# Kernel optimization log

Hardware: AMD Instinct MI355X
Metric: run time of the kernel (lower is better)

The kernel has to match this reference:

```python
import jax, jax.numpy as jnp
import numpy as np

NCLASSES = 80
MAX_BOXES = 100
IOU_THR = 0.5
SCORE_THR = 0.0
NEG = -1e9


def arrange_bbox(xy, wh):
    # xy, wh: [1, H, W, 3, 2]
    H, W = xy.shape[1], xy.shape[2]
    gx, gy = jnp.meshgrid(jnp.arange(W), jnp.arange(H))  # 'xy' indexing, each [H, W]
    grid = jnp.stack([gx, gy], axis=-1)[:, :, None, :].astype(xy.dtype)  # [H, W, 1, 2]
    gsize = jnp.array([H, W], dtype=xy.dtype)  # TF divides last dim [x, y] by [H, W]
    xy = (xy + grid) / gsize
    return jnp.concatenate([xy - wh / 2, xy + wh / 2], axis=-1)  # [1,H,W,3,4]


def hard_nms(boxes, scores):
    # boxes: [N,4] (x1,y1,x2,y2); scores: [N]. Greedy NMS, fixed MAX_BOXES output.
    areas = (boxes[:, 2] - boxes[:, 0]) * (boxes[:, 3] - boxes[:, 1])  # [N]

    def step(sw, _):
        j = jnp.argmax(sw)
        s = sw[j]
        valid = s > SCORE_THR
        bj = boxes[j]
        iw = jnp.clip(jnp.minimum(boxes[:, 2], bj[2]) - jnp.maximum(boxes[:, 0], bj[0]), 0.0)
        ih = jnp.clip(jnp.minimum(boxes[:, 3], bj[3]) - jnp.maximum(boxes[:, 1], bj[1]), 0.0)
        inter = iw * ih
        iou = inter / (areas + areas[j] - inter)
        sw = jnp.where((iou > IOU_THR) & valid, NEG, sw)  # suppresses j itself too
        return sw, (jnp.where(valid, j, -1), jnp.where(valid, s, 0.0), valid)

    _, (sel_idx, sel_scores, valids) = jax.lax.scan(step, scores, None, length=MAX_BOXES)
    return sel_idx, sel_scores, valids


def decode(grid0, grid1, grid2, anchors_table):
    outs = (grid0, grid1, grid2)
    anch = (anchors_table[2], anchors_table[1], anchors_table[0])
    bbs, confs, probs = [], [], []
    for g, a in zip(outs, anch):
        xy, wh, obj, cp = jnp.split(g, [2, 4, 5], axis=-1)
        b = arrange_bbox(xy, jnp.exp(wh) * a)
        bbs.append(b.reshape(1, -1, 4))
        confs.append(obj.reshape(1, -1, 1))
        probs.append(cp.reshape(1, -1, NCLASSES))
    bbox = jnp.concatenate(bbs, axis=1).reshape(-1, 4)          # [N,4]
    conf = jnp.concatenate(confs, axis=1)[0, :, 0]              # [N]
    cp = jnp.concatenate(probs, axis=1)[0]                      # [N,C]
    cls_idx = jnp.argmax(cp, axis=-1)                           # [N]
    maxprob = jnp.max(cp, axis=-1)                              # [N]
    # TF code broadcasts conf[1,N,1]*maxprob[N] -> [N,N], then reduce_max over axis 1.
    # Mathematically: scores[i] = max_j conf[i]*maxprob[j] = max(conf*max(mp), conf*min(mp)).
    scores = jnp.maximum(conf * jnp.max(maxprob), conf * jnp.min(maxprob))
    return bbox, scores, cls_idx


def reference(grid0, grid1, grid2, anchors_table):
    bbox, scores, cls_idx = decode(grid0, grid1, grid2, anchors_table)
    sel_idx, sel_scores, valids = hard_nms(bbox, scores)
    safe = jnp.clip(sel_idx, 0)
    sel_boxes = jnp.where(valids[:, None], bbox[safe], 0.0)[None]      # [1,MAX,4]
    sel_scores = sel_scores[None]                                       # [1,MAX]
    sel_classes = jnp.where(valids, cls_idx[safe], 0)[None]            # [1,MAX]
    num_valid = jnp.sum(valids).astype(jnp.int32)[None]                # [1]
    return sel_boxes, sel_scores, sel_classes, num_valid


def setup_inputs() -> dict:
    key = jax.random.key(0)
    k0, k1, k2 = jax.random.split(key, 3)
    grid0 = jax.random.normal(k0, (1, 48, 48, 3, 85), jnp.float32)
    grid1 = jax.random.normal(k1, (1, 96, 96, 3, 85), jnp.float32)
    grid2 = jax.random.normal(k2, (1, 192, 192, 3, 85), jnp.float32)
    anchors = np.array([[[10, 13], [16, 30], [33, 23]],
                        [[30, 61], [62, 45], [59, 119]],
                        [[116, 90], [156, 198], [373, 326]]], np.float32) / 416.0
    return {"grid0": grid0, "grid1": grid1, "grid2": grid2,
            "anchors_table": jnp.asarray(anchors)}
```

## Files before the change

kernel.cpp:

```cpp
#include <hip/hip_runtime.h>
#include <hip/hip_bf16.h>
#include <math.h>


#define NCLS  80
#define MAXB  100
#define N0    6912
#define N1    27648
#define NTOT  145152
#define NTILE 2268
#define NB    4096
#define CAP   2048
#define CAPL  2048
#define CHUNK 256
#define NEGF  -3.402823466e38f
#define POSF   3.402823466e38f

#define WS_CONF 0
#define WS_SCAL (NTOT * 4)
#define WS_PART (WS_SCAL + 16)
#define WS_HIST (WS_PART + NTILE * 16)
#define WS_BINC (WS_HIST + 8 * NB * 4)
#define WS_SUF  (WS_BINC + NB * 4)
#define WS_META (WS_SUF + (NB + 2) * 4)
#define WS_CAND (WS_META + 16)

__device__ __forceinline__ int binOf(float s, float Smax) {
    int b = (int)((s / Smax) * (float)NB);
    return b > (NB - 1) ? (NB - 1) : b;
}
__device__ __forceinline__ float smaxOf(const float* scal) {
    float Mx = scal[0], Mn = scal[1], cmx = scal[2], cmn = scal[3];
    return fmaxf(fmaxf(cmx * Mx, cmx * Mn), fmaxf(cmn * Mx, cmn * Mn));
}
__device__ __forceinline__ float rdlane(float v, int l) {
    return __uint_as_float(__builtin_amdgcn_readlane(__float_as_uint(v), l));
}
__device__ __forceinline__ void decodeBox(int idx, const float* __restrict__ g0,
        const float* __restrict__ g1, const float* __restrict__ g2,
        const float* __restrict__ anch,
        float& x1, float& y1, float& x2, float& y2) {
    const float* g; int H, ar, j;
    if (idx < N0)           { g = g0; H = 48;  ar = 2; j = idx; }
    else if (idx < N0 + N1) { g = g1; H = 96;  ar = 1; j = idx - N0; }
    else                    { g = g2; H = 192; ar = 0; j = idx - N0 - N1; }
    const float* r = g + (size_t)j * 85;
    float tx = r[0], ty = r[1], tw = r[2], th = r[3];
    int cell = j / 3, a = j - cell * 3;
    int hh = cell / H, ww = cell - hh * H;
    float xc = (tx + (float)ww) / (float)H;
    float yc = (ty + (float)hh) / (float)H;
    float bw = expf(tw) * anch[ar * 6 + a * 2];
    float bh = expf(th) * anch[ar * 6 + a * 2 + 1];
    x1 = xc - bw * 0.5f; y1 = yc - bh * 0.5f;
    x2 = xc + bw * 0.5f; y2 = yc + bh * 0.5f;
}

__global__ __launch_bounds__(256) void k_decode(
        const float* __restrict__ g0, const float* __restrict__ g1,
        const float* __restrict__ g2, float* __restrict__ conf,
        float* __restrict__ part) {
    __shared__ float sm[5440];
    __shared__ float red[16];
    const int tid = threadIdx.x;
    const int tile = blockIdx.x;
    const float* p; int ibase, lt;
    if (tile < 108)      { p = g0; ibase = 0;       lt = tile; }
    else if (tile < 540) { p = g1; ibase = N0;      lt = tile - 108; }
    else                 { p = g2; ibase = N0 + N1; lt = tile - 540; }
    const float4* src = (const float4*)(p + (size_t)lt * 5440);
    for (int w = tid; w < 1360; w += 256) ((float4*)sm)[w] = src[w];
    __syncthreads();

    const int b = tid >> 2, pp = tid & 3;
    const float* row = sm + b * 85;
    float best = row[5 + pp * 20];
    #pragma unroll
    for (int k = 1; k < 20; k++) best = fmaxf(best, row[5 + pp * 20 + k]);
    best = fmaxf(best, __shfl_xor(best, 1));
    best = fmaxf(best, __shfl_xor(best, 2));
    float cmx = NEGF, cmn = POSF;
    if (pp == 0) {
        float obj = row[4];
        conf[ibase + lt * 64 + b] = obj;
        cmx = obj; cmn = obj;
    }
    float mpmax = best, mpmin = best;
    for (int off = 32; off; off >>= 1) {
        mpmax = fmaxf(mpmax, __shfl_down(mpmax, off));
        mpmin = fminf(mpmin, __shfl_down(mpmin, off));
        cmx   = fmaxf(cmx,   __shfl_down(cmx,   off));
        cmn   = fminf(cmn,   __shfl_down(cmn,   off));
    }
    const int lane = tid & 63, wid = tid >> 6;
    if (lane == 0) {
        red[wid * 4 + 0] = mpmax; red[wid * 4 + 1] = mpmin;
        red[wid * 4 + 2] = cmx;   red[wid * 4 + 3] = cmn;
    }
    __syncthreads();
    if (tid == 0) {
        float a0 = red[0], a1 = red[1], a2 = red[2], a3 = red[3];
        for (int w = 1; w < 4; w++) {
            a0 = fmaxf(a0, red[w * 4 + 0]); a1 = fminf(a1, red[w * 4 + 1]);
            a2 = fmaxf(a2, red[w * 4 + 2]); a3 = fminf(a3, red[w * 4 + 3]);
        }
        part[tile * 4 + 0] = a0; part[tile * 4 + 1] = a1;
        part[tile * 4 + 2] = a2; part[tile * 4 + 3] = a3;
    }
}

__global__ __launch_bounds__(256) void k_reduce(const float* __restrict__ part,
                                                float* __restrict__ scal) {
    __shared__ float red[16];
    const int tid = threadIdx.x;
    float a0 = NEGF, a1 = POSF, a2 = NEGF, a3 = POSF;
    for (int b = tid; b < NTILE; b += 256) {
        float4 p4 = ((const float4*)part)[b];
        a0 = fmaxf(a0, p4.x); a1 = fminf(a1, p4.y);
        a2 = fmaxf(a2, p4.z); a3 = fminf(a3, p4.w);
    }
    for (int off = 32; off; off >>= 1) {
        a0 = fmaxf(a0, __shfl_down(a0, off)); a1 = fminf(a1, __shfl_down(a1, off));
        a2 = fmaxf(a2, __shfl_down(a2, off)); a3 = fminf(a3, __shfl_down(a3, off));
    }
    const int lane = tid & 63, wid = tid >> 6;
    if (lane == 0) {
        red[wid * 4 + 0] = a0; red[wid * 4 + 1] = a1;
        red[wid * 4 + 2] = a2; red[wid * 4 + 3] = a3;
    }
    __syncthreads();
    if (tid == 0) {
        for (int w = 1; w < 4; w++) {
            a0 = fmaxf(a0, red[w * 4 + 0]); a1 = fminf(a1, red[w * 4 + 1]);
            a2 = fmaxf(a2, red[w * 4 + 2]); a3 = fminf(a3, red[w * 4 + 3]);
        }
        scal[0] = a0; scal[1] = a1; scal[2] = a2; scal[3] = a3;
    }
}

__global__ __launch_bounds__(256) void k_hist(const float* __restrict__ conf,
                                              const float* __restrict__ scal,
                                              int* __restrict__ hist) {
    int i = blockIdx.x * 256 + threadIdx.x;
    float Mx = scal[0], Mn = scal[1];
    float Smax = smaxOf(scal);
    float c = conf[i];
    float s = fmaxf(c * Mx, c * Mn);
    if (s > 0.0f && Smax > 0.0f)
        atomicAdd(&hist[((blockIdx.x & 7) << 12) + binOf(s, Smax)], 1);
}

__global__ __launch_bounds__(1024) void k_thresh(const int* __restrict__ hist,
                                                 int* __restrict__ suf,
                                                 int* __restrict__ meta) {
    __shared__ int grp[1024];
    const int tid = threadIdx.x;
    int b0 = tid * 4;
    int h[4];
    #pragma unroll
    for (int q = 0; q < 4; q++) {
        int s = 0;
        #pragma unroll
        for (int sh = 0; sh < 8; sh++) s += hist[sh * NB + b0 + q];
        h[q] = s;
    }
    grp[tid] = h[0] + h[1] + h[2] + h[3];
    __syncthreads();
    for (int d = 1; d < 1024; d <<= 1) {
        int add = (tid + d < 1024) ? grp[tid + d] : 0;
        __syncthreads();
        grp[tid] += add;
        __syncthreads();
    }
    int gnext = (tid + 1 < 1024) ? grp[tid + 1] : 0;
    suf[b0 + 3] = gnext + h[3];
    suf[b0 + 2] = gnext + h[3] + h[2];
    suf[b0 + 1] = gnext + h[3] + h[2] + h[1];
    suf[b0 + 0] = gnext + h[3] + h[2] + h[1] + h[0];
    if (tid == 0) suf[NB] = 0;
    __syncthreads();
    if (tid == 0) {
        int L = 0, R = NB - 1, res = NB - 1;
        while (L <= R) {
            int m = (L + R) >> 1;
            if (suf[m] <= CAP) { res = m; R = m - 1; } else L = m + 1;
        }
        meta[0] = res;
    }
}

__global__ __launch_bounds__(256) void k_compact(
        const float* __restrict__ conf, const float* __restrict__ scal,
        const int* __restrict__ suf, const int* __restrict__ meta,
        int* __restrict__ binCtr, unsigned long long* __restrict__ cand) {
    int i = blockIdx.x * 256 + threadIdx.x;
    float Mx = scal[0], Mn = scal[1];
    float Smax = smaxOf(scal);
    float c = conf[i];
    float s = fmaxf(c * Mx, c * Mn);
    int lo = meta[0];
    if (s > 0.0f && Smax > 0.0f) {
        int b = binOf(s, Smax);
        if (b >= lo) {
            int pos = suf[b + 1] + atomicAdd(&binCtr[b], 1);
            if (pos < CAP)
                cand[pos] = ((unsigned long long)__float_as_uint(s) << 32)
                          | (unsigned long long)(~(unsigned)i);
        }
    }
}

__global__ __launch_bounds__(64) void k_nms(
        const float* __restrict__ g0, const float* __restrict__ g1,
        const float* __restrict__ g2, const float* __restrict__ anch,
        const float* __restrict__ conf, const float* __restrict__ scal,
        const int* __restrict__ suf, const int* __restrict__ meta,
        const unsigned long long* __restrict__ cand, float* __restrict__ out) {
    __shared__ unsigned long long keys[CAPL];
    __shared__ float selX1[MAXB], selY1[MAXB], selX2[MAXB], selY2[MAXB],
                     selA[MAXB], selS[MAXB];
    __shared__ int selIdx[MAXB];
    __shared__ int sh_cnt;

    const int lane = threadIdx.x;
    const float Mx = scal[0], Mn = scal[1];
    const float Smax = smaxOf(scal);
    const int loGlob = meta[0];
    int nsel = 0;
    int hi = NB;

    while (nsel < MAXB && hi > 0) {
        const bool fast = hi > loGlob;
        const int sufHi = suf[hi];
        int l;
        {
            int lb = fast ? loGlob : 0;
            int capHere = fast ? CHUNK : CAPL;
            int L = lb, R = hi - 1, res = hi - 1;
            while (L <= R) {
                int m = (L + R) >> 1;
                if (suf[m] - sufHi <= capHere) { res = m; R = m - 1; } else L = m + 1;
            }
            l = res;
        }
        int cnt;
        if (fast) {
            cnt = suf[l] - sufHi;
            for (int i = lane; i < cnt; i += 64) keys[i] = cand[sufHi + i];
        } else {
            if (lane == 0) sh_cnt = 0;
            __syncthreads();
            for (int i = lane; i < NTOT; i += 64) {
                float c = conf[i];
                float s = fmaxf(c * Mx, c * Mn);
                if (s > 0.0f) {
                    int b = binOf(s, Smax);
                    if (b >= l && b < hi) {
                        int pos = atomicAdd(&sh_cnt, 1);
                        if (pos < CAPL)
                            keys[pos] = ((unsigned long long)__float_as_uint(s) << 32)
                                      | (unsigned long long)(~(unsigned)i);
                    }
                }
            }
            __syncthreads();
            cnt = sh_cnt; if (cnt > CAPL) cnt = CAPL;
        }
        if (cnt > 0) {
            int n = 2; while (n < cnt) n <<= 1;
            for (int i = cnt + lane; i < n; i += 64) keys[i] = 0ULL;
            __syncthreads();
            for (int k = 2; k <= n; k <<= 1) {
                for (int j = k >> 1; j > 0; j >>= 1) {
                    int half = n >> 1;
                    for (int t = lane; t < half; t += 64) {
                        int i = ((t & ~(j - 1)) << 1) | (t & (j - 1));
                        int ixj = i | j;
                        unsigned long long ka = keys[i], kb = keys[ixj];
                        if ((ka < kb) == ((i & k) == 0)) { keys[i] = kb; keys[ixj] = ka; }
                    }
                    __syncthreads();
                }
            }
            for (int bpos = 0; bpos < cnt && nsel < MAXB; bpos += 64) {
                int t = bpos + lane;
                bool alive = (t < cnt);
                float x1 = 0.f, y1 = 0.f, x2 = 0.f, y2 = 0.f, area = 0.f, sc = 0.f;
                int idx = 0;
                if (alive) {
                    unsigned long long key = keys[t];
                    idx = (int)(~(unsigned)key);
                    sc = __uint_as_float((unsigned)(key >> 32));
                    decodeBox(idx, g0, g1, g2, anch, x1, y1, x2, y2);
                    area = (x2 - x1) * (y2 - y1);
                    for (int s2 = 0; s2 < nsel; s2++) {
                        float iw = fminf(x2, selX2[s2]) - fmaxf(x1, selX1[s2]);
                        float ih = fminf(y2, selY2[s2]) - fmaxf(y1, selY1[s2]);
                        iw = fmaxf(iw, 0.f); ih = fmaxf(ih, 0.f);
                        float inter = iw * ih;
                        if (inter / (area + selA[s2] - inter) > 0.5f) { alive = false; break; }
                    }
                }
                while (nsel < MAXB) {
                    unsigned long long bal = __ballot(alive);
                    if (!bal) break;
                    int w = __ffsll((unsigned long long)bal) - 1;
                    float wx1 = rdlane(x1, w), wy1 = rdlane(y1, w);
                    float wx2 = rdlane(x2, w), wy2 = rdlane(y2, w);
                    float wa  = rdlane(area, w);
                    if (lane == w) {
                        selX1[nsel] = x1; selY1[nsel] = y1;
                        selX2[nsel] = x2; selY2[nsel] = y2;
                        selA[nsel] = area; selS[nsel] = sc; selIdx[nsel] = idx;
                    }
                    if (alive) {
                        float iw = fminf(x2, wx2) - fmaxf(x1, wx1);
                        float ih = fminf(y2, wy2) - fmaxf(y1, wy1);
                        iw = fmaxf(iw, 0.f); ih = fmaxf(ih, 0.f);
                        float inter = iw * ih;
                        if (inter / (area + wa - inter) > 0.5f) alive = false;
                    }
                    nsel++;
                }
                __syncthreads();
            }
        }
        hi = l;
    }
    __syncthreads();

    for (int k = lane; k < MAXB; k += 64) {
        float b0 = 0.f, b1 = 0.f, b2 = 0.f, b3 = 0.f, sv = 0.f, cv = 0.f;
        if (k < nsel) {
            b0 = selX1[k]; b1 = selY1[k]; b2 = selX2[k]; b3 = selY2[k];
            sv = selS[k];
            int idx = selIdx[k];
            const float* g; int j;
            if (idx < N0)           { g = g0; j = idx; }
            else if (idx < N0 + N1) { g = g1; j = idx - N0; }
            else                    { g = g2; j = idx - N0 - N1; }
            const float* r = g + (size_t)j * 85 + 5;
            float v[NCLS];
            #pragma unroll
            for (int q = 0; q < NCLS; q++) v[q] = r[q];
            float best = v[0]; int c = 0;
            #pragma unroll
            for (int q = 1; q < NCLS; q++)
                if (v[q] > best) { best = v[q]; c = q; }
            cv = (float)c;
        }
        out[4 * k + 0] = b0; out[4 * k + 1] = b1;
        out[4 * k + 2] = b2; out[4 * k + 3] = b3;
        out[400 + k] = sv;
        out[500 + k] = cv;
    }
    if (lane == 0) out[600] = (float)nsel;
}

extern "C" void kernel_launch(void* const* d_in, const int* in_sizes, int n_in,
                              void* d_out, int out_size, void* d_ws, size_t ws_size,
                              hipStream_t stream) {
    const float* g0   = (const float*)d_in[0];
    const float* g1   = (const float*)d_in[1];
    const float* g2   = (const float*)d_in[2];
    const float* anch = (const float*)d_in[3];
    char* ws = (char*)d_ws;
    float* conf  = (float*)(ws + WS_CONF);
    float* scal  = (float*)(ws + WS_SCAL);
    float* part  = (float*)(ws + WS_PART);
    int*   hist  = (int*)(ws + WS_HIST);
    int*   binc  = (int*)(ws + WS_BINC);
    int*   suf   = (int*)(ws + WS_SUF);
    int*   meta  = (int*)(ws + WS_META);
    unsigned long long* cand = (unsigned long long*)(ws + WS_CAND);
    float* out   = (float*)d_out;

    hipMemsetAsync(ws + WS_HIST, 0, 9 * NB * 4, stream);
    k_decode <<<NTILE, 256, 0, stream>>>(g0, g1, g2, conf, part);
    k_reduce <<<1, 256, 0, stream>>>(part, scal);
    k_hist   <<<NTOT / 256, 256, 0, stream>>>(conf, scal, hist);
    k_thresh <<<1, 1024, 0, stream>>>(hist, suf, meta);
    k_compact<<<NTOT / 256, 256, 0, stream>>>(conf, scal, suf, meta, binc, cand);
    k_nms    <<<1, 64, 0, stream>>>(g0, g1, g2, anch, conf, scal, suf, meta, cand, out);
}
```

Before: 161.3 us.

## Fold memset and reduce into neighbouring kernels, precompute NMS chunk boundaries, keep selected boxes in registers

Removes the hipMemsetAsync and the single-block k_reduce launch. Histogram zeroing moves into k_decode, and each k_hist block redundantly reduces the per-tile partials itself. k_thresh now also computes the global scalars and a ladder of four thresholds (256..2048), so k_nms can load its candidate chunks directly without per-chunk binary searches. Selected boxes are held in wave registers and read with readlane instead of from shared memory. The cost is redundant partial reductions in every hist block and more register pressure in the NMS kernel.

Measured after the change: 167.2 us. 1.04x slower.

```diff
diff --git a/kernel.cpp b/kernel.cpp
--- a/kernel.cpp
+++ b/kernel.cpp
@@ -9,10 +9,10 @@
 #define N1    27648
 #define NTOT  145152
 #define NTILE 2268
+#define NHB   567
 #define NB    4096
 #define CAP   2048
 #define CAPL  2048
-#define CHUNK 256
 #define NEGF  -3.402823466e38f
 #define POSF   3.402823466e38f
 
@@ -22,16 +22,12 @@
 #define WS_HIST (WS_PART + NTILE * 16)
 #define WS_BINC (WS_HIST + 8 * NB * 4)
 #define WS_SUF  (WS_BINC + NB * 4)
-#define WS_META (WS_SUF + (NB + 2) * 4)
+#define WS_META (WS_SUF + (NB + 4) * 4)
 #define WS_CAND (WS_META + 16)
 
 __device__ __forceinline__ int binOf(float s, float Smax) {
     int b = (int)((s / Smax) * (float)NB);
     return b > (NB - 1) ? (NB - 1) : b;
-}
-__device__ __forceinline__ float smaxOf(const float* scal) {
-    float Mx = scal[0], Mn = scal[1], cmx = scal[2], cmn = scal[3];
-    return fmaxf(fmaxf(cmx * Mx, cmx * Mn), fmaxf(cmn * Mx, cmn * Mn));
 }
 __device__ __forceinline__ float rdlane(float v, int l) {
     return __uint_as_float(__builtin_amdgcn_readlane(__float_as_uint(v), l));
@@ -59,11 +55,12 @@
 __global__ __launch_bounds__(256) void k_decode(
         const float* __restrict__ g0, const float* __restrict__ g1,
         const float* __restrict__ g2, float* __restrict__ conf,
-        float* __restrict__ part) {
+        float* __restrict__ part, int* __restrict__ histAll) {
     __shared__ float sm[5440];
     __shared__ float red[16];
     const int tid = threadIdx.x;
     const int tile = blockIdx.x;
+    if (tile < 144) histAll[tile * 256 + tid] = 0;
     const float* p; int ibase, lt;
     if (tile < 108)      { p = g0; ibase = 0;       lt = tile; }
     else if (tile < 540) { p = g1; ibase = N0;      lt = tile - 108; }
@@ -109,10 +106,11 @@
     }
 }
 
-__global__ __launch_bounds__(256) void k_reduce(const float* __restrict__ part,
-                                                float* __restrict__ scal) {
+__global__ __launch_bounds__(256) void k_hist(const float* __restrict__ conf,
+                                              const float* __restrict__ part,
+                                              int* __restrict__ hist) {
     __shared__ float red[16];
-    const int tid = threadIdx.x;
+    const int tid = threadIdx.x, lane = tid & 63, wid = tid >> 6;
     float a0 = NEGF, a1 = POSF, a2 = NEGF, a3 = POSF;
     for (int b = tid; b < NTILE; b += 256) {
         float4 p4 = ((const float4*)part)[b];
@@ -123,46 +121,52 @@
         a0 = fmaxf(a0, __shfl_down(a0, off)); a1 = fminf(a1, __shfl_down(a1, off));
         a2 = fmaxf(a2, __shfl_down(a2, off)); a3 = fminf(a3, __shfl_down(a3, off));
     }
-    const int lane = tid & 63, wid = tid >> 6;
     if (lane == 0) {
         red[wid * 4 + 0] = a0; red[wid * 4 + 1] = a1;
         red[wid * 4 + 2] = a2; red[wid * 4 + 3] = a3;
     }
     __syncthreads();
-    if (tid == 0) {
-        for (int w = 1; w < 4; w++) {
-            a0 = fmaxf(a0, red[w * 4 + 0]); a1 = fminf(a1, red[w * 4 + 1]);
-            a2 = fmaxf(a2, red[w * 4 + 2]); a3 = fminf(a3, red[w * 4 + 3]);
-        }
-        scal[0] = a0; scal[1] = a1; scal[2] = a2; scal[3] = a3;
-    }
-}
-
-__global__ __launch_bounds__(256) void k_hist(const float* __restrict__ conf,
-                                              const float* __restrict__ scal,
-                                              int* __restrict__ hist) {
-    int i = blockIdx.x * 256 + threadIdx.x;
-    float Mx = scal[0], Mn = scal[1];
-    float Smax = smaxOf(scal);
+    float Mx = fmaxf(fmaxf(red[0], red[4]),  fmaxf(red[8],  red[12]));
+    float Mn = fminf(fminf(red[1], red[5]),  fminf(red[9],  red[13]));
+    float cx = fmaxf(fmaxf(red[2], red[6]),  fmaxf(red[10], red[14]));
+    float cn = fminf(fminf(red[3], red[7]),  fminf(red[11], red[15]));
+    float Smax = fmaxf(fmaxf(cx * Mx, cx * Mn), fmaxf(cn * Mx, cn * Mn));
+    int i = blockIdx.x * 256 + tid;
     float c = conf[i];
     float s = fmaxf(c * Mx, c * Mn);
     if (s > 0.0f && Smax > 0.0f)
         atomicAdd(&hist[((blockIdx.x & 7) << 12) + binOf(s, Smax)], 1);
 }
 
-__global__ __launch_bounds__(1024) void k_thresh(const int* __restrict__ hist,
-                                                 int* __restrict__ suf,
-                                                 int* __restrict__ meta) {
+__global__ __launch_bounds__(1024) void k_thresh(
+        const int* __restrict__ hist, const float* __restrict__ part,
+        int* __restrict__ suf, int* __restrict__ meta, float* __restrict__ scal) {
     __shared__ int grp[1024];
-    const int tid = threadIdx.x;
+    __shared__ int sufL[NB + 1];
+    __shared__ float red[64];
+    const int tid = threadIdx.x, lane = tid & 63, wid = tid >> 6;
+    float a0 = NEGF, a1 = POSF, a2 = NEGF, a3 = POSF;
+    for (int b = tid; b < NTILE; b += 1024) {
+        float4 p4 = ((const float4*)part)[b];
+        a0 = fmaxf(a0, p4.x); a1 = fminf(a1, p4.y);
+        a2 = fmaxf(a2, p4.z); a3 = fminf(a3, p4.w);
+    }
+    for (int off = 32; off; off >>= 1) {
+        a0 = fmaxf(a0, __shfl_down(a0, off)); a1 = fminf(a1, __shfl_down(a1, off));
+        a2 = fmaxf(a2, __shfl_down(a2, off)); a3 = fminf(a3, __shfl_down(a3, off));
+    }
+    if (lane == 0) {
+        red[wid * 4 + 0] = a0; red[wid * 4 + 1] = a1;
+        red[wid * 4 + 2] = a2; red[wid * 4 + 3] = a3;
+    }
     int b0 = tid * 4;
     int h[4];
     #pragma unroll
     for (int q = 0; q < 4; q++) {
-        int s = 0;
+        int ss = 0;
         #pragma unroll
-        for (int sh = 0; sh < 8; sh++) s += hist[sh * NB + b0 + q];
-        h[q] = s;
+        for (int sh = 0; sh < 8; sh++) ss += hist[sh * NB + b0 + q];
+        h[q] = ss;
     }
     grp[tid] = h[0] + h[1] + h[2] + h[3];
     __syncthreads();
@@ -173,19 +177,27 @@
         __syncthreads();
     }
     int gnext = (tid + 1 < 1024) ? grp[tid + 1] : 0;
-    suf[b0 + 3] = gnext + h[3];
-    suf[b0 + 2] = gnext + h[3] + h[2];
-    suf[b0 + 1] = gnext + h[3] + h[2] + h[1];
-    suf[b0 + 0] = gnext + h[3] + h[2] + h[1] + h[0];
-    if (tid == 0) suf[NB] = 0;
-    __syncthreads();
-    if (tid == 0) {
+    int v3 = gnext + h[3], v2 = v3 + h[2], v1 = v2 + h[1], v0 = v1 + h[0];
+    sufL[b0] = v0; sufL[b0 + 1] = v1; sufL[b0 + 2] = v2; sufL[b0 + 3] = v3;
+    suf[b0] = v0;  suf[b0 + 1] = v1;  suf[b0 + 2] = v2;  suf[b0 + 3] = v3;
+    if (tid == 0) { sufL[NB] = 0; suf[NB] = 0; }
+    __syncthreads();
+    if (tid < 4) {
+        int cap = 256 << tid;
         int L = 0, R = NB - 1, res = NB - 1;
         while (L <= R) {
             int m = (L + R) >> 1;
-            if (suf[m] <= CAP) { res = m; R = m - 1; } else L = m + 1;
-        }
-        meta[0] = res;
+            if (sufL[m] <= cap) { res = m; R = m - 1; } else L = m + 1;
+        }
+        meta[tid == 3 ? 0 : tid + 1] = res;
+    }
+    if (tid == 4) {
+        float m0 = red[0], m1 = red[1], m2 = red[2], m3 = red[3];
+        for (int w = 1; w < 16; w++) {
+            m0 = fmaxf(m0, red[w * 4 + 0]); m1 = fminf(m1, red[w * 4 + 1]);
+            m2 = fmaxf(m2, red[w * 4 + 2]); m3 = fminf(m3, red[w * 4 + 3]);
+        }
+        scal[0] = m0; scal[1] = m1; scal[2] = m2; scal[3] = m3;
     }
 }
 
@@ -194,8 +206,8 @@
         const int* __restrict__ suf, const int* __restrict__ meta,
         int* __restrict__ binCtr, unsigned long long* __restrict__ cand) {
     int i = blockIdx.x * 256 + threadIdx.x;
-    float Mx = scal[0], Mn = scal[1];
-    float Smax = smaxOf(scal);
+    float Mx = scal[0], Mn = scal[1], cx = scal[2], cn = scal[3];
+    float Smax = fmaxf(fmaxf(cx * Mx, cx * Mn), fmaxf(cn * Mx, cn * Mn));
     float c = conf[i];
     float s = fmaxf(c * Mx, c * Mn);
     int lo = meta[0];
@@ -217,115 +229,146 @@
         const int* __restrict__ suf, const int* __restrict__ meta,
         const unsigned long long* __restrict__ cand, float* __restrict__ out) {
     __shared__ unsigned long long keys[CAPL];
-    __shared__ float selX1[MAXB], selY1[MAXB], selX2[MAXB], selY2[MAXB],
-                     selA[MAXB], selS[MAXB];
+    __shared__ float selX1[MAXB], selY1[MAXB], selX2[MAXB], selY2[MAXB], selS[MAXB];
     __shared__ int selIdx[MAXB];
     __shared__ int sh_cnt;
 
     const int lane = threadIdx.x;
-    const float Mx = scal[0], Mn = scal[1];
-    const float Smax = smaxOf(scal);
-    const int loGlob = meta[0];
+    float4 sc4 = *(const float4*)scal;
+    const float Mx = sc4.x, Mn = sc4.y;
+    const float Smax = fmaxf(fmaxf(sc4.z * Mx, sc4.z * Mn),
+                             fmaxf(sc4.w * Mx, sc4.w * Mn));
+    int4 mt = *(const int4*)meta;
+    int ladMine = 0;
+    if (lane == 1) ladMine = mt.y; else if (lane == 2) ladMine = mt.z;
+    else if (lane == 3) ladMine = mt.w; else if (lane == 4) ladMine = mt.x;
+    int sufMine = (lane >= 1 && lane <= 4) ? suf[ladMine] : 0;
+    const int sufA1 = __builtin_amdgcn_readlane(sufMine, 1);
+    const int sufA2 = __builtin_amdgcn_readlane(sufMine, 2);
+    const int sufA3 = __builtin_amdgcn_readlane(sufMine, 3);
+    const int sufA4 = __builtin_amdgcn_readlane(sufMine, 4);
+
     int nsel = 0;
-    int hi = NB;
-
-    while (nsel < MAXB && hi > 0) {
-        const bool fast = hi > loGlob;
-        const int sufHi = suf[hi];
-        int l;
-        {
-            int lb = fast ? loGlob : 0;
-            int capHere = fast ? CHUNK : CAPL;
-            int L = lb, R = hi - 1, res = hi - 1;
-            while (L <= R) {
-                int m = (L + R) >> 1;
-                if (suf[m] - sufHi <= capHere) { res = m; R = m - 1; } else L = m + 1;
-            }
-            l = res;
-        }
-        int cnt;
-        if (fast) {
-            cnt = suf[l] - sufHi;
-            for (int i = lane; i < cnt; i += 64) keys[i] = cand[sufHi + i];
-        } else {
-            if (lane == 0) sh_cnt = 0;
-            __syncthreads();
-            for (int i = lane; i < NTOT; i += 64) {
-                float c = conf[i];
-                float s = fmaxf(c * Mx, c * Mn);
-                if (s > 0.0f) {
-                    int b = binOf(s, Smax);
-                    if (b >= l && b < hi) {
-                        int pos = atomicAdd(&sh_cnt, 1);
-                        if (pos < CAPL)
-                            keys[pos] = ((unsigned long long)__float_as_uint(s) << 32)
-                                      | (unsigned long long)(~(unsigned)i);
-                    }
-                }
-            }
-            __syncthreads();
-            cnt = sh_cnt; if (cnt > CAPL) cnt = CAPL;
-        }
-        if (cnt > 0) {
-            int n = 2; while (n < cnt) n <<= 1;
-            for (int i = cnt + lane; i < n; i += 64) keys[i] = 0ULL;
-            __syncthreads();
-            for (int k = 2; k <= n; k <<= 1) {
-                for (int j = k >> 1; j > 0; j >>= 1) {
-                    int half = n >> 1;
-                    for (int t = lane; t < half; t += 64) {
-                        int i = ((t & ~(j - 1)) << 1) | (t & (j - 1));
-                        int ixj = i | j;
-                        unsigned long long ka = keys[i], kb = keys[ixj];
-                        if ((ka < kb) == ((i & k) == 0)) { keys[i] = kb; keys[ixj] = ka; }
-                    }
-                    __syncthreads();
-                }
-            }
-            for (int bpos = 0; bpos < cnt && nsel < MAXB; bpos += 64) {
-                int t = bpos + lane;
-                bool alive = (t < cnt);
-                float x1 = 0.f, y1 = 0.f, x2 = 0.f, y2 = 0.f, area = 0.f, sc = 0.f;
-                int idx = 0;
-                if (alive) {
-                    unsigned long long key = keys[t];
-                    idx = (int)(~(unsigned)key);
-                    sc = __uint_as_float((unsigned)(key >> 32));
-                    decodeBox(idx, g0, g1, g2, anch, x1, y1, x2, y2);
-                    area = (x2 - x1) * (y2 - y1);
-                    for (int s2 = 0; s2 < nsel; s2++) {
-                        float iw = fminf(x2, selX2[s2]) - fmaxf(x1, selX1[s2]);
-                        float ih = fminf(y2, selY2[s2]) - fmaxf(y1, selY1[s2]);
-                        iw = fmaxf(iw, 0.f); ih = fmaxf(ih, 0.f);
-                        float inter = iw * ih;
-                        if (inter / (area + selA[s2] - inter) > 0.5f) { alive = false; break; }
-                    }
-                }
-                while (nsel < MAXB) {
-                    unsigned long long bal = __ballot(alive);
-                    if (!bal) break;
-                    int w = __ffsll((unsigned long long)bal) - 1;
-                    float wx1 = rdlane(x1, w), wy1 = rdlane(y1, w);
-                    float wx2 = rdlane(x2, w), wy2 = rdlane(y2, w);
-                    float wa  = rdlane(area, w);
-                    if (lane == w) {
-                        selX1[nsel] = x1; selY1[nsel] = y1;
-                        selX2[nsel] = x2; selY2[nsel] = y2;
-                        selA[nsel] = area; selS[nsel] = sc; selIdx[nsel] = idx;
-                    }
-                    if (alive) {
-                        float iw = fminf(x2, wx2) - fmaxf(x1, wx1);
-                        float ih = fminf(y2, wy2) - fmaxf(y1, wy1);
-                        iw = fmaxf(iw, 0.f); ih = fmaxf(ih, 0.f);
-                        float inter = iw * ih;
-                        if (inter / (area + wa - inter) > 0.5f) alive = false;
-                    }
-                    nsel++;
+    float s0x1 = 0, s0y1 = 0, s0x2 = 0, s0y2 = 0, s0a = 0;
+    float s1x1 = 0, s1y1 = 0, s1x2 = 0, s1y2 = 0, s1a = 0;
+
+    auto sortDesc = [&](int cnt) {
+        int n = 2; while (n < cnt) n <<= 1;
+        for (int i = cnt + lane; i < n; i += 64) keys[i] = 0ULL;
+        __syncthreads();
+        for (int k = 2; k <= n; k <<= 1) {
+            for (int j = k >> 1; j > 0; j >>= 1) {
+                int half = n >> 1;
+                for (int t = lane; t < half; t += 64) {
+                    int i = ((t & ~(j - 1)) << 1) | (t & (j - 1));
+                    int ixj = i | j;
+                    unsigned long long ka = keys[i], kb = keys[ixj];
+                    if ((ka < kb) == ((i & k) == 0)) { keys[i] = kb; keys[ixj] = ka; }
                 }
                 __syncthreads();
             }
         }
-        hi = l;
+    };
+
+    auto sweep = [&](int cnt) {
+        for (int bpos = 0; bpos < cnt && nsel < MAXB; bpos += 64) {
+            int t = bpos + lane;
+            bool alive = (t < cnt);
+            float x1 = 0, y1 = 0, x2 = 0, y2 = 0, area = 0, sc = 0;
+            int idx = 0;
+            if (alive) {
+                unsigned long long key = keys[t];
+                idx = (int)(~(unsigned)key);
+                sc = __uint_as_float((unsigned)(key >> 32));
+                decodeBox(idx, g0, g1, g2, anch, x1, y1, x2, y2);
+                area = (x2 - x1) * (y2 - y1);
+            }
+            for (int s2 = 0; s2 < nsel; s2++) {
+                float wx1, wy1, wx2, wy2, wa;
+                if (s2 < 64) {
+                    wx1 = rdlane(s0x1, s2); wy1 = rdlane(s0y1, s2);
+                    wx2 = rdlane(s0x2, s2); wy2 = rdlane(s0y2, s2);
+                    wa  = rdlane(s0a,  s2);
+                } else {
+                    int q = s2 - 64;
+                    wx1 = rdlane(s1x1, q); wy1 = rdlane(s1y1, q);
+                    wx2 = rdlane(s1x2, q); wy2 = rdlane(s1y2, q);
+                    wa  = rdlane(s1a,  q);
+                }
+                if (alive) {
+                    float iw = fmaxf(fminf(x2, wx2) - fmaxf(x1, wx1), 0.f);
+                    float ih = fmaxf(fminf(y2, wy2) - fmaxf(y1, wy1), 0.f);
+                    float inter = iw * ih;
+                    if (inter / (area + wa - inter) > 0.5f) alive = false;
+                }
+            }
+            while (nsel < MAXB) {
+                unsigned long long bal = __ballot(alive);
+                if (!bal) break;
+                int w = __ffsll(bal) - 1;
+                float wx1 = rdlane(x1, w), wy1 = rdlane(y1, w);
+                float wx2 = rdlane(x2, w), wy2 = rdlane(y2, w);
+                float wa  = rdlane(area, w);
+                if (lane == w) {
+                    selX1[nsel] = x1; selY1[nsel] = y1;
+                    selX2[nsel] = x2; selY2[nsel] = y2;
+                    selS[nsel] = sc; selIdx[nsel] = idx;
+                }
+                if (nsel < 64) {
+                    if (lane == nsel) { s0x1 = wx1; s0y1 = wy1; s0x2 = wx2; s0y2 = wy2; s0a = wa; }
+                } else {
+                    if (lane == nsel - 64) { s1x1 = wx1; s1y1 = wy1; s1x2 = wx2; s1y2 = wy2; s1a = wa; }
+                }
+                if (alive) {
+                    float iw = fmaxf(fminf(x2, wx2) - fmaxf(x1, wx1), 0.f);
+                    float ih = fmaxf(fminf(y2, wy2) - fmaxf(y1, wy1), 0.f);
+                    float inter = iw * ih;
+                    if (inter / (area + wa - inter) > 0.5f) alive = false;
+                }
+                nsel++;
+            }
+        }
+    };
+
+    int bases[4] = { 0, sufA1, sufA2, sufA3 };
+    int ends[4]  = { sufA1, sufA2, sufA3, sufA4 };
+    #pragma unroll
+    for (int c = 0; c < 4; c++) {
+        if (nsel >= MAXB) break;
+        int base = bases[c], cnt = ends[c] - base;
+        if (cnt <= 0) continue;
+        for (int i = lane; i < cnt; i += 64) keys[i] = cand[base + i];
+        sortDesc(cnt);
+        sweep(cnt);
+    }
+    int hi = mt.x, sufHi = sufA4;
+    while (nsel < MAXB && hi > 0) {
+        int L = 0, R = hi - 1, res = hi - 1, resV = 0;
+        while (L <= R) {
+            int m = (L + R) >> 1;
+            int v = suf[m];
+            if (v - sufHi <= CAPL) { res = m; resV = v; R = m - 1; } else L = m + 1;
+        }
+        int l = res;
+        if (lane == 0) sh_cnt = 0;
+        __syncthreads();
+        for (int i = lane; i < NTOT; i += 64) {
+            float c = conf[i];
+            float s = fmaxf(c * Mx, c * Mn);
+            if (s > 0.0f && Smax > 0.0f) {
+                int b = binOf(s, Smax);
+                if (b >= l && b < hi) {
+                    int pos = atomicAdd(&sh_cnt, 1);
+                    if (pos < CAPL)
+                        keys[pos] = ((unsigned long long)__float_as_uint(s) << 32)
+                                  | (unsigned long long)(~(unsigned)i);
+                }
+            }
+        }
+        __syncthreads();
+        int cnt = sh_cnt; if (cnt > CAPL) cnt = CAPL;
+        if (cnt > 0) { sortDesc(cnt); sweep(cnt); }
+        hi = l; sufHi = resV;
     }
     __syncthreads();
 
@@ -375,11 +418,9 @@
     unsigned long long* cand = (unsigned long long*)(ws + WS_CAND);
     float* out   = (float*)d_out;
 
-    hipMemsetAsync(ws + WS_HIST, 0, 9 * NB * 4, stream);
-    k_decode <<<NTILE, 256, 0, stream>>>(g0, g1, g2, conf, part);
-    k_reduce <<<1, 256, 0, stream>>>(part, scal);
-    k_hist   <<<NTOT / 256, 256, 0, stream>>>(conf, scal, hist);
-    k_thresh <<<1, 1024, 0, stream>>>(hist, suf, meta);
-    k_compact<<<NTOT / 256, 256, 0, stream>>>(conf, scal, suf, meta, binc, cand);
+    k_decode <<<NTILE, 256, 0, stream>>>(g0, g1, g2, conf, part, hist);
+    k_hist   <<<NHB, 256, 0, stream>>>(conf, part, hist);
+    k_thresh <<<1, 1024, 0, stream>>>(hist, part, suf, meta, scal);
+    k_compact<<<NHB, 256, 0, stream>>>(conf, scal, suf, meta, binc, cand);
     k_nms    <<<1, 64, 0, stream>>>(g0, g1, g2, anch, conf, scal, suf, meta, cand, out);
 }
```
